# Kernel tuning notes

Measured on AMD Instinct MI355X. Metric: run time of the kernel, lower is better.

## Reference

```python
import jax, jax.numpy as jnp
import numpy as np

EMBED_DIM = 128
NUM_HEADS = 16
D_K = EMBED_DIM // NUM_HEADS  # must equal n_wires = 8


def setup_inputs() -> dict:
    key = jax.random.key(0)
    k1, k2 = jax.random.split(key)
    x = jax.random.normal(k1, (8, 2048, EMBED_DIM), dtype=jnp.float32)
    theta = jax.random.normal(k2, (D_K,), dtype=jnp.float32)  # trainable RX angles, one per wire
    return {"x": x, "theta": theta}


def _quantum_measure(q, theta):
    # q: [B, H, S, 8]. RX(x)RX(theta) = RX(x+theta); product state gives <Z_i> = cos(phi_i).
    # CNOT chain C(0,1)..C(6,7),C(7,0) in Heisenberg picture:
    #   <Z_0> = prod_{i=1..7} cos(phi_i);  <Z_w> = prod_{i=0..w} cos(phi_i), w>=1.
    c = jnp.cos(q + theta)                       # [B,H,S,8]
    cp = jnp.cumprod(c, axis=-1)                 # prefix products prod_{0..w}
    z0 = jnp.prod(c[..., 1:], axis=-1, keepdims=True)
    return jnp.concatenate([z0, cp[..., 1:]], axis=-1)  # [B,H,S,8]


def reference(x, theta):
    B, S, E = x.shape
    # split heads: [B,S,E] -> [B,H,S,d_k]
    q = x.reshape(B, S, NUM_HEADS, D_K).transpose(0, 2, 1, 3)
    out = _quantum_measure(q, theta)             # [B,H,S,8]
    # merge heads back: [B,S,E]
    out = out.transpose(0, 2, 1, 3).reshape(B, S, E)
    scores = jnp.einsum('bse,bte->bst', out, out) / jnp.sqrt(jnp.float32(D_K))
    attn = jax.nn.softmax(scores, axis=-1)       # dropout = identity in eval mode
    return jnp.einsum('bst,bte->bse', attn, out)
```

## Files before the change

### kernel.cpp

```cpp
#include <hip/hip_runtime.h>

#define NB 8
#define SS 2048
#define DD 128
#define SCALE2 0.5101817664764817f
#define NEGINF -3.0e38f

typedef _Float16 f16x8 __attribute__((ext_vector_type(8)));
typedef float f32x16 __attribute__((ext_vector_type(16)));
typedef unsigned short u16;
typedef u16 u16x8 __attribute__((ext_vector_type(8)));

__device__ __forceinline__ unsigned pkrtz(float a, float b) {
    unsigned w;
    asm("v_cvt_pkrtz_f16_f32 %0, %1, %2" : "=v"(w) : "v"(a), "v"(b));
    return w;
}

__global__ __launch_bounds__(512) void qmeasure_kernel(const float* __restrict__ x,
                                                       const float* __restrict__ theta,
                                                       u16* __restrict__ G1,
                                                       u16* __restrict__ G2) {
    __shared__ u16 olds[32][136];
    const int bid = blockIdx.x;
    const int b = bid & 7;
    const int t = bid >> 3;
    const int tid = threadIdx.x;
    const int s = tid >> 4;
    const int c = tid & 15;

    float th[8];
    *(float4*)th = *(const float4*)theta;
    *(float4*)(th + 4) = *(const float4*)(theta + 4);

    const float* xp = x + (((size_t)b * SS + t * 32 + s) * DD) + c * 8;
    float4 a = *(const float4*)xp;
    float4 a2 = *(const float4*)(xp + 4);
    float cc[8];
    cc[0] = __cosf(a.x + th[0]);  cc[1] = __cosf(a.y + th[1]);
    cc[2] = __cosf(a.z + th[2]);  cc[3] = __cosf(a.w + th[3]);
    cc[4] = __cosf(a2.x + th[4]); cc[5] = __cosf(a2.y + th[5]);
    cc[6] = __cosf(a2.z + th[6]); cc[7] = __cosf(a2.w + th[7]);
    float o[8];
    o[1] = cc[0] * cc[1];
    o[2] = o[1] * cc[2]; o[3] = o[2] * cc[3]; o[4] = o[3] * cc[4];
    o[5] = o[4] * cc[5]; o[6] = o[5] * cc[6]; o[7] = o[6] * cc[7];
    float z = cc[1] * cc[2]; z *= cc[3]; z *= cc[4]; z *= cc[5]; z *= cc[6]; z *= cc[7];
    o[0] = z;

    u16x8 w;
#pragma unroll
    for (int e = 0; e < 8; ++e) w[e] = __builtin_bit_cast(u16, (_Float16)o[e]);
    *(u16x8*)&olds[s][c * 8] = w;
    __syncthreads();

    {
        const int kc = tid >> 6, hh = (tid >> 5) & 1, r = tid & 31;
        u16x8 g;
#pragma unroll
        for (int u = 0; u < 8; ++u) g[u] = olds[r][kc * 16 + hh * 8 + u];
        *(u16x8*)(G1 + (size_t)b * (SS * DD) + ((size_t)t * 512 + tid) * 8) = g;
    }
    {
        const int lo5 = tid & 31;
        const int hh = (tid >> 5) & 1;
        const int dkc = tid >> 6;
        const int dt = dkc >> 1, kc2 = dkc & 1;
        u16x8 g;
#pragma unroll
        for (int u = 0; u < 8; ++u) g[u] = olds[kc2 * 16 + hh * 8 + u][dt * 32 + lo5];
        const int chunk = t * 512 + dkc * 64 + hh * 32 + lo5;
        *(u16x8*)(G2 + (size_t)b * (SS * DD) + (size_t)chunk * 8) = g;
    }
}


struct SMState { float m, l; };

__device__ __forceinline__ void tile_step(const f16x8* __restrict__ kf,
                                          const f16x8* __restrict__ vf,
                                          const f16x8* __restrict__ qf,
                                          f32x16* __restrict__ accT,
                                          float& m, float& l) {
    f32x16 acc;
#pragma unroll
    for (int e = 0; e < 16; ++e) acc[e] = 0.f;
    __builtin_amdgcn_s_setprio(1);
#pragma unroll
    for (int kc = 0; kc < 8; ++kc)
        acc = __builtin_amdgcn_mfma_f32_32x32x16_f16(kf[kc], qf[kc], acc, 0, 0, 0);
    __builtin_amdgcn_s_setprio(0);

    float ma = fmaxf(fmaxf(acc[0], acc[1]), acc[2]);
    float mb = fmaxf(fmaxf(acc[8], acc[9]), acc[10]);
    ma = fmaxf(fmaxf(ma, acc[3]), acc[4]);
    mb = fmaxf(fmaxf(mb, acc[11]), acc[12]);
    ma = fmaxf(fmaxf(ma, acc[5]), acc[6]);
    mb = fmaxf(fmaxf(mb, acc[13]), acc[14]);
    ma = fmaxf(fmaxf(ma, acc[7]), mb);
    float tmax = fmaxf(ma, acc[15]) * SCALE2;
    tmax = fmaxf(tmax, __shfl_xor(tmax, 32));
    if (!__all(tmax <= m + 8.f)) {
        const float mnew = fmaxf(m, tmax);
        const float corr = exp2f(m - mnew);
        l *= corr;
#pragma unroll
        for (int dt = 0; dt < 4; ++dt)
#pragma unroll
            for (int e = 0; e < 16; ++e) accT[dt][e] *= corr;
        m = mnew;
    }
#pragma unroll
    for (int r = 0; r < 16; ++r) acc[r] = exp2f(acc[r] * SCALE2 - m);
    float s0 = (acc[0] + acc[1]) + (acc[2] + acc[3]);
    float s1 = (acc[4] + acc[5]) + (acc[6] + acc[7]);
    float s2 = (acc[8] + acc[9]) + (acc[10] + acc[11]);
    float s3 = (acc[12] + acc[13]) + (acc[14] + acc[15]);
    float rowsum = (s0 + s1) + (s2 + s3);
    rowsum += __shfl_xor(rowsum, 32);
    l += rowsum;

    f16x8 pa[2];
#pragma unroll
    for (int kc2 = 0; kc2 < 2; ++kc2) {
        const int r0 = kc2 * 8;
        unsigned w0 = pkrtz(acc[r0 + 0], acc[r0 + 1]);
        unsigned w2 = pkrtz(acc[r0 + 4], acc[r0 + 5]);
        asm("v_permlane32_swap_b32 %0, %1" : "+v"(w0), "+v"(w2));
        unsigned w1 = pkrtz(acc[r0 + 2], acc[r0 + 3]);
        unsigned w3 = pkrtz(acc[r0 + 6], acc[r0 + 7]);
        asm("v_permlane32_swap_b32 %0, %1" : "+v"(w1), "+v"(w3));
        union { unsigned w[4]; f16x8 v; } u;
        u.w[0] = w0; u.w[1] = w1; u.w[2] = w2; u.w[3] = w3;
        pa[kc2] = u.v;
    }

    __builtin_amdgcn_s_setprio(1);
#pragma unroll
    for (int dt = 0; dt < 4; ++dt) {
        f32x16 a = accT[dt];
        a = __builtin_amdgcn_mfma_f32_32x32x16_f16(vf[dt * 2 + 0], pa[0], a, 0, 0, 0);
        a = __builtin_amdgcn_mfma_f32_32x32x16_f16(vf[dt * 2 + 1], pa[1], a, 0, 0, 0);
        accT[dt] = a;
    }
    __builtin_amdgcn_s_setprio(0);
}

__global__ __launch_bounds__(512, 2) void qattn_kernel(const u16* __restrict__ G1g,
                                                       const u16* __restrict__ G2g,
                                                       float* __restrict__ out) {
    __shared__ float obuf[2][3][2][16][64];
    __shared__ float mlb[2][3][2][32];

    const int tid = threadIdx.x;
    const int lane = tid & 63;
    const int wave = tid >> 6;
    const int lo5 = lane & 31;
    const int hi = lane >> 5;
    const int qw = wave & 1;
    const int kq = wave >> 1;
    const int bid = blockIdx.x;
    const int b = bid & 7;
    const int qg = bid >> 3;

    const u16* G1b = G1g + (size_t)b * (SS * DD);
    const u16* G2b = G2g + (size_t)b * (SS * DD);

    f16x8 qf[8];
    {
        const u16* qp = G1b + (size_t)(qg * 2 + qw) * 4096 + lane * 8;
#pragma unroll
        for (int kc = 0; kc < 8; ++kc) qf[kc] = *(const f16x8*)(qp + kc * 512);
    }

    f32x16 accT[4];
#pragma unroll
    for (int dt = 0; dt < 4; ++dt)
#pragma unroll
        for (int e = 0; e < 16; ++e) accT[dt][e] = 0.f;
    float m = NEGINF, l = 0.f;

    f16x8 kfA[8], kfB[8], vf[8];
    {
        const u16* kp = G1b + (size_t)(kq * 16) * 4096 + lane * 8;
#pragma unroll
        for (int j = 0; j < 8; ++j) kfA[j] = *(const f16x8*)(kp + j * 512);
    }

    for (int it2 = 0; it2 < 8; ++it2) {
        const int t0 = kq * 16 + it2 * 2;
        {
            const u16* vp = G2b + (size_t)t0 * 4096 + lane * 8;
#pragma unroll
            for (int j = 0; j < 8; ++j) vf[j] = *(const f16x8*)(vp + j * 512);
            const u16* np = G1b + (size_t)(t0 + 1) * 4096 + lane * 8;
#pragma unroll
            for (int j = 0; j < 8; ++j) kfB[j] = *(const f16x8*)(np + j * 512);
            tile_step(kfA, vf, qf, accT, m, l);
        }
        {
            const u16* vp = G2b + (size_t)(t0 + 1) * 4096 + lane * 8;
#pragma unroll
            for (int j = 0; j < 8; ++j) vf[j] = *(const f16x8*)(vp + j * 512);
            if (it2 < 7) {
                const u16* np = G1b + (size_t)(t0 + 2) * 4096 + lane * 8;
#pragma unroll
                for (int j = 0; j < 8; ++j) kfA[j] = *(const f16x8*)(np + j * 512);
            }
            tile_step(kfB, vf, qf, accT, m, l);
        }
    }

    __syncthreads();
    float* orow = out + ((size_t)b * SS + qg * 64 + qw * 32 + lo5) * DD;
#pragma unroll
    for (int half = 0; half < 2; ++half) {
        if (kq > 0) {
            if (half == 0 && hi == 0) {
                mlb[qw][kq - 1][0][lo5] = m;
                mlb[qw][kq - 1][1][lo5] = l;
            }
#pragma unroll
            for (int dh = 0; dh < 2; ++dh)
#pragma unroll
                for (int r = 0; r < 16; ++r)
                    obuf[qw][kq - 1][dh][r][lane] = accT[half * 2 + dh][r];
        }
        __syncthreads();
        if (kq == 0) {
            const float mj0 = mlb[qw][0][0][lo5], lj0 = mlb[qw][0][1][lo5];
            const float mj1 = mlb[qw][1][0][lo5], lj1 = mlb[qw][1][1][lo5];
            const float mj2 = mlb[qw][2][0][lo5], lj2 = mlb[qw][2][1][lo5];
            const float ms = fmaxf(fmaxf(m, mj0), fmaxf(mj1, mj2));
            const float w0 = exp2f(m - ms), w1 = exp2f(mj0 - ms);
            const float w2 = exp2f(mj1 - ms), w3 = exp2f(mj2 - ms);
            const float linv = 1.f / (l * w0 + lj0 * w1 + lj1 * w2 + lj2 * w3);
#pragma unroll
            for (int dh = 0; dh < 2; ++dh) {
                const int dt = half * 2 + dh;
#pragma unroll
                for (int r = 0; r < 16; ++r) {
                    const float o = accT[dt][r] * w0 + obuf[qw][0][dh][r][lane] * w1 +
                                    obuf[qw][1][dh][r][lane] * w2 + obuf[qw][2][dh][r][lane] * w3;
                    const int drow = (r & 3) + 8 * (r >> 2) + 4 * hi;
                    orow[dt * 32 + drow] = o * linv;
                }
            }
        }
        __syncthreads();
    }
}

extern "C" void kernel_launch(void* const* d_in, const int* in_sizes, int n_in,
                              void* d_out, int out_size, void* d_ws, size_t ws_size,
                              hipStream_t stream) {
    const float* x = (const float*)d_in[0];
    const float* theta = (const float*)d_in[1];
    float* outp = (float*)d_out;
    u16* G1 = (u16*)d_ws;
    u16* G2 = G1 + (size_t)NB * SS * DD;

    qmeasure_kernel<<<512, 512, 0, stream>>>(x, theta, G1, G2);
    qattn_kernel<<<256, 512, 0, stream>>>(G1, G2, outp);
}
```

Measured before the change: 37.86 us.

## Split attention into 4-wave blocks per 32-query tile and drop K/V register prefetch

The attention kernel now launches 512 blocks of 256 threads, each handling one 32-query tile with four waves splitting the key range, instead of 256 blocks of 512 threads covering two query tiles. The explicit double-buffered K register prefetch is removed, and K/V fragments are loaded inline next to their MFMAs, which lowers register pressure so occupancy can rise (launch bounds 256,4). The cross-wave combine is done in a single pass using a larger shared buffer rather than two halves. The trade-off is that global load latency is hidden less by software pipelining and must come from more resident waves instead.

```diff
diff --git a/kernel.cpp b/kernel.cpp
--- a/kernel.cpp
+++ b/kernel.cpp
@@ -10,9 +10,10 @@
 typedef float f32x16 __attribute__((ext_vector_type(16)));
 typedef unsigned short u16;
 typedef u16 u16x8 __attribute__((ext_vector_type(8)));
-
-__device__ __forceinline__ unsigned pkrtz(float a, float b) {
-    unsigned w;
+typedef unsigned int u32;
+
+__device__ __forceinline__ u32 pkrtz(float a, float b) {
+    u32 w;
     asm("v_cvt_pkrtz_f16_f32 %0, %1, %2" : "=v"(w) : "v"(a), "v"(b));
     return w;
 }
@@ -74,101 +75,28 @@
     }
 }
 
-
-struct SMState { float m, l; };
-
-__device__ __forceinline__ void tile_step(const f16x8* __restrict__ kf,
-                                          const f16x8* __restrict__ vf,
-                                          const f16x8* __restrict__ qf,
-                                          f32x16* __restrict__ accT,
-                                          float& m, float& l) {
-    f32x16 acc;
-#pragma unroll
-    for (int e = 0; e < 16; ++e) acc[e] = 0.f;
-    __builtin_amdgcn_s_setprio(1);
-#pragma unroll
-    for (int kc = 0; kc < 8; ++kc)
-        acc = __builtin_amdgcn_mfma_f32_32x32x16_f16(kf[kc], qf[kc], acc, 0, 0, 0);
-    __builtin_amdgcn_s_setprio(0);
-
-    float ma = fmaxf(fmaxf(acc[0], acc[1]), acc[2]);
-    float mb = fmaxf(fmaxf(acc[8], acc[9]), acc[10]);
-    ma = fmaxf(fmaxf(ma, acc[3]), acc[4]);
-    mb = fmaxf(fmaxf(mb, acc[11]), acc[12]);
-    ma = fmaxf(fmaxf(ma, acc[5]), acc[6]);
-    mb = fmaxf(fmaxf(mb, acc[13]), acc[14]);
-    ma = fmaxf(fmaxf(ma, acc[7]), mb);
-    float tmax = fmaxf(ma, acc[15]) * SCALE2;
-    tmax = fmaxf(tmax, __shfl_xor(tmax, 32));
-    if (!__all(tmax <= m + 8.f)) {
-        const float mnew = fmaxf(m, tmax);
-        const float corr = exp2f(m - mnew);
-        l *= corr;
-#pragma unroll
-        for (int dt = 0; dt < 4; ++dt)
-#pragma unroll
-            for (int e = 0; e < 16; ++e) accT[dt][e] *= corr;
-        m = mnew;
-    }
-#pragma unroll
-    for (int r = 0; r < 16; ++r) acc[r] = exp2f(acc[r] * SCALE2 - m);
-    float s0 = (acc[0] + acc[1]) + (acc[2] + acc[3]);
-    float s1 = (acc[4] + acc[5]) + (acc[6] + acc[7]);
-    float s2 = (acc[8] + acc[9]) + (acc[10] + acc[11]);
-    float s3 = (acc[12] + acc[13]) + (acc[14] + acc[15]);
-    float rowsum = (s0 + s1) + (s2 + s3);
-    rowsum += __shfl_xor(rowsum, 32);
-    l += rowsum;
-
-    f16x8 pa[2];
-#pragma unroll
-    for (int kc2 = 0; kc2 < 2; ++kc2) {
-        const int r0 = kc2 * 8;
-        unsigned w0 = pkrtz(acc[r0 + 0], acc[r0 + 1]);
-        unsigned w2 = pkrtz(acc[r0 + 4], acc[r0 + 5]);
-        asm("v_permlane32_swap_b32 %0, %1" : "+v"(w0), "+v"(w2));
-        unsigned w1 = pkrtz(acc[r0 + 2], acc[r0 + 3]);
-        unsigned w3 = pkrtz(acc[r0 + 6], acc[r0 + 7]);
-        asm("v_permlane32_swap_b32 %0, %1" : "+v"(w1), "+v"(w3));
-        union { unsigned w[4]; f16x8 v; } u;
-        u.w[0] = w0; u.w[1] = w1; u.w[2] = w2; u.w[3] = w3;
-        pa[kc2] = u.v;
-    }
-
-    __builtin_amdgcn_s_setprio(1);
-#pragma unroll
-    for (int dt = 0; dt < 4; ++dt) {
-        f32x16 a = accT[dt];
-        a = __builtin_amdgcn_mfma_f32_32x32x16_f16(vf[dt * 2 + 0], pa[0], a, 0, 0, 0);
-        a = __builtin_amdgcn_mfma_f32_32x32x16_f16(vf[dt * 2 + 1], pa[1], a, 0, 0, 0);
-        accT[dt] = a;
-    }
-    __builtin_amdgcn_s_setprio(0);
-}
-
-__global__ __launch_bounds__(512, 2) void qattn_kernel(const u16* __restrict__ G1g,
+__global__ __launch_bounds__(256, 4) void qattn_kernel(const u16* __restrict__ G1g,
                                                        const u16* __restrict__ G2g,
                                                        float* __restrict__ out) {
-    __shared__ float obuf[2][3][2][16][64];
-    __shared__ float mlb[2][3][2][32];
+    __shared__ float obuf[3][4][16][64];
+    __shared__ float mlb[3][2][32];
 
     const int tid = threadIdx.x;
     const int lane = tid & 63;
-    const int wave = tid >> 6;
+    const int kq = tid >> 6;
     const int lo5 = lane & 31;
     const int hi = lane >> 5;
-    const int qw = wave & 1;
-    const int kq = wave >> 1;
     const int bid = blockIdx.x;
     const int b = bid & 7;
-    const int qg = bid >> 3;
+    const int qt = bid >> 3;
+    const int lane8 = lane * 8;
 
     const u16* G1b = G1g + (size_t)b * (SS * DD);
     const u16* G2b = G2g + (size_t)b * (SS * DD);
 
     f16x8 qf[8];
     {
-        const u16* qp = G1b + (size_t)(qg * 2 + qw) * 4096 + lane * 8;
+        const u16* qp = G1b + (size_t)qt * 4096 + lane8;
 #pragma unroll
         for (int kc = 0; kc < 8; ++kc) qf[kc] = *(const f16x8*)(qp + kc * 512);
     }
@@ -180,74 +108,109 @@
         for (int e = 0; e < 16; ++e) accT[dt][e] = 0.f;
     float m = NEGINF, l = 0.f;
 
-    f16x8 kfA[8], kfB[8], vf[8];
-    {
-        const u16* kp = G1b + (size_t)(kq * 16) * 4096 + lane * 8;
-#pragma unroll
-        for (int j = 0; j < 8; ++j) kfA[j] = *(const f16x8*)(kp + j * 512);
-    }
-
-    for (int it2 = 0; it2 < 8; ++it2) {
-        const int t0 = kq * 16 + it2 * 2;
-        {
-            const u16* vp = G2b + (size_t)t0 * 4096 + lane * 8;
-#pragma unroll
-            for (int j = 0; j < 8; ++j) vf[j] = *(const f16x8*)(vp + j * 512);
-            const u16* np = G1b + (size_t)(t0 + 1) * 4096 + lane * 8;
-#pragma unroll
-            for (int j = 0; j < 8; ++j) kfB[j] = *(const f16x8*)(np + j * 512);
-            tile_step(kfA, vf, qf, accT, m, l);
-        }
-        {
-            const u16* vp = G2b + (size_t)(t0 + 1) * 4096 + lane * 8;
-#pragma unroll
-            for (int j = 0; j < 8; ++j) vf[j] = *(const f16x8*)(vp + j * 512);
-            if (it2 < 7) {
-                const u16* np = G1b + (size_t)(t0 + 2) * 4096 + lane * 8;
-#pragma unroll
-                for (int j = 0; j < 8; ++j) kfA[j] = *(const f16x8*)(np + j * 512);
+    for (int it = 0; it < 16; ++it) {
+        const int t = kq * 16 + it;
+        const u16* kp = G1b + (size_t)t * 4096 + lane8;
+        const u16* vp = G2b + (size_t)t * 4096 + lane8;
+
+        f32x16 acc;
+#pragma unroll
+        for (int e = 0; e < 16; ++e) acc[e] = 0.f;
+        __builtin_amdgcn_s_setprio(1);
+#pragma unroll
+        for (int kc = 0; kc < 8; ++kc) {
+            f16x8 kf = *(const f16x8*)(kp + kc * 512);
+            acc = __builtin_amdgcn_mfma_f32_32x32x16_f16(kf, qf[kc], acc, 0, 0, 0);
+        }
+        __builtin_amdgcn_s_setprio(0);
+
+        float ma = fmaxf(fmaxf(acc[0], acc[1]), acc[2]);
+        float mb = fmaxf(fmaxf(acc[8], acc[9]), acc[10]);
+        ma = fmaxf(fmaxf(ma, acc[3]), acc[4]);
+        mb = fmaxf(fmaxf(mb, acc[11]), acc[12]);
+        ma = fmaxf(fmaxf(ma, acc[5]), acc[6]);
+        mb = fmaxf(fmaxf(mb, acc[13]), acc[14]);
+        ma = fmaxf(fmaxf(ma, acc[7]), mb);
+        float tmax = fmaxf(ma, acc[15]) * SCALE2;
+        tmax = fmaxf(tmax, __shfl_xor(tmax, 32));
+        if (!__all(tmax <= m + 8.f)) {
+            const float mnew = fmaxf(m, tmax);
+            const float corr = exp2f(m - mnew);
+            l *= corr;
+#pragma unroll
+            for (int dt = 0; dt < 4; ++dt)
+#pragma unroll
+                for (int e = 0; e < 16; ++e) accT[dt][e] *= corr;
+            m = mnew;
+        }
+#pragma unroll
+        for (int r = 0; r < 16; ++r) acc[r] = exp2f(acc[r] * SCALE2 - m);
+        float s0 = (acc[0] + acc[1]) + (acc[2] + acc[3]);
+        float s1 = (acc[4] + acc[5]) + (acc[6] + acc[7]);
+        float s2 = (acc[8] + acc[9]) + (acc[10] + acc[11]);
+        float s3 = (acc[12] + acc[13]) + (acc[14] + acc[15]);
+        float rowsum = (s0 + s1) + (s2 + s3);
+        rowsum += __shfl_xor(rowsum, 32);
+        l += rowsum;
+
+        f16x8 pa[2];
+#pragma unroll
+        for (int kc2 = 0; kc2 < 2; ++kc2) {
+            const int r0 = kc2 * 8;
+            u32 w0 = pkrtz(acc[r0 + 0], acc[r0 + 1]);
+            u32 w2 = pkrtz(acc[r0 + 4], acc[r0 + 5]);
+            asm("v_permlane32_swap_b32 %0, %1" : "+v"(w0), "+v"(w2));
+            u32 w1 = pkrtz(acc[r0 + 2], acc[r0 + 3]);
+            u32 w3 = pkrtz(acc[r0 + 6], acc[r0 + 7]);
+            asm("v_permlane32_swap_b32 %0, %1" : "+v"(w1), "+v"(w3));
+            union { u32 w[4]; f16x8 v; } u;
+            u.w[0] = w0; u.w[1] = w1; u.w[2] = w2; u.w[3] = w3;
+            pa[kc2] = u.v;
+        }
+
+        __builtin_amdgcn_s_setprio(1);
+#pragma unroll
+        for (int dt = 0; dt < 4; ++dt) {
+            f16x8 vf0 = *(const f16x8*)(vp + (dt * 2 + 0) * 512);
+            f16x8 vf1 = *(const f16x8*)(vp + (dt * 2 + 1) * 512);
+            f32x16 a = accT[dt];
+            a = __builtin_amdgcn_mfma_f32_32x32x16_f16(vf0, pa[0], a, 0, 0, 0);
+            a = __builtin_amdgcn_mfma_f32_32x32x16_f16(vf1, pa[1], a, 0, 0, 0);
+            accT[dt] = a;
+        }
+        __builtin_amdgcn_s_setprio(0);
+    }
+
+    if (kq > 0) {
+        if (hi == 0) {
+            mlb[kq - 1][0][lo5] = m;
+            mlb[kq - 1][1][lo5] = l;
+        }
+#pragma unroll
+        for (int dt = 0; dt < 4; ++dt)
+#pragma unroll
+            for (int r = 0; r < 16; ++r)
+                obuf[kq - 1][dt][r][lane] = accT[dt][r];
+    }
+    __syncthreads();
+    if (kq == 0) {
+        const float mj0 = mlb[0][0][lo5], lj0 = mlb[0][1][lo5];
+        const float mj1 = mlb[1][0][lo5], lj1 = mlb[1][1][lo5];
+        const float mj2 = mlb[2][0][lo5], lj2 = mlb[2][1][lo5];
+        const float ms = fmaxf(fmaxf(m, mj0), fmaxf(mj1, mj2));
+        const float w0 = exp2f(m - ms), w1 = exp2f(mj0 - ms);
+        const float w2 = exp2f(mj1 - ms), w3 = exp2f(mj2 - ms);
+        const float linv = 1.f / (l * w0 + lj0 * w1 + lj1 * w2 + lj2 * w3);
+        float* orow = out + ((size_t)b * SS + qt * 32 + lo5) * DD;
+#pragma unroll
+        for (int dt = 0; dt < 4; ++dt)
+#pragma unroll
+            for (int r = 0; r < 16; ++r) {
+                const float o = accT[dt][r] * w0 + obuf[0][dt][r][lane] * w1 +
+                                obuf[1][dt][r][lane] * w2 + obuf[2][dt][r][lane] * w3;
+                const int drow = (r & 3) + 8 * (r >> 2) + 4 * hi;
+                orow[dt * 32 + drow] = o * linv;
             }
-            tile_step(kfB, vf, qf, accT, m, l);
-        }
-    }
-
-    __syncthreads();
-    float* orow = out + ((size_t)b * SS + qg * 64 + qw * 32 + lo5) * DD;
-#pragma unroll
-    for (int half = 0; half < 2; ++half) {
-        if (kq > 0) {
-            if (half == 0 && hi == 0) {
-                mlb[qw][kq - 1][0][lo5] = m;
-                mlb[qw][kq - 1][1][lo5] = l;
-            }
-#pragma unroll
-            for (int dh = 0; dh < 2; ++dh)
-#pragma unroll
-                for (int r = 0; r < 16; ++r)
-                    obuf[qw][kq - 1][dh][r][lane] = accT[half * 2 + dh][r];
-        }
-        __syncthreads();
-        if (kq == 0) {
-            const float mj0 = mlb[qw][0][0][lo5], lj0 = mlb[qw][0][1][lo5];
-            const float mj1 = mlb[qw][1][0][lo5], lj1 = mlb[qw][1][1][lo5];
-            const float mj2 = mlb[qw][2][0][lo5], lj2 = mlb[qw][2][1][lo5];
-            const float ms = fmaxf(fmaxf(m, mj0), fmaxf(mj1, mj2));
-            const float w0 = exp2f(m - ms), w1 = exp2f(mj0 - ms);
-            const float w2 = exp2f(mj1 - ms), w3 = exp2f(mj2 - ms);
-            const float linv = 1.f / (l * w0 + lj0 * w1 + lj1 * w2 + lj2 * w3);
-#pragma unroll
-            for (int dh = 0; dh < 2; ++dh) {
-                const int dt = half * 2 + dh;
-#pragma unroll
-                for (int r = 0; r < 16; ++r) {
-                    const float o = accT[dt][r] * w0 + obuf[qw][0][dh][r][lane] * w1 +
-                                    obuf[qw][1][dh][r][lane] * w2 + obuf[qw][2][dh][r][lane] * w3;
-                    const int drow = (r & 3) + 8 * (r >> 2) + 4 * hi;
-                    orow[dt * 32 + drow] = o * linv;
-                }
-            }
-        }
-        __syncthreads();
     }
 }
 
@@ -261,5 +224,5 @@
     u16* G2 = G1 + (size_t)NB * SS * DD;
 
     qmeasure_kernel<<<512, 512, 0, stream>>>(x, theta, G1, G2);
-    qattn_kernel<<<256, 512, 0, stream>>>(G1, G2, outp);
-}
+    qattn_kernel<<<512, 256, 0, stream>>>(G1, G2, outp);
+}
```

Result: slower. 40.25 us (+6.3%).
